# Optimization experiments

Hardware: AMD Instinct MI355X
Metric: run time of the kernel (lower is better)

Reference implementation:

```python
import jax, jax.numpy as jnp
import numpy as np

NUM_HEADS = 12

def _get_rel_pos(size, rel_pos):
    # q_size == k_size == size, no interpolation needed (table has 2*size-1 rows)
    idx = jnp.arange(size)[:, None] - jnp.arange(size)[None, :] + (size - 1)  # (size,size)
    return rel_pos[idx]  # (size, size, head_dim)

def setup_inputs() -> dict:
    key = jax.random.key(0)
    ks = jax.random.split(key, 7)
    B, H, W, dim = 8, 32, 32, 768
    head_dim = dim // NUM_HEADS
    return {
        "x": jax.random.normal(ks[0], (B, H, W, dim), jnp.float32),
        "qkv_w": jax.random.normal(ks[1], (dim, 3 * dim), jnp.float32) * 0.02,
        "qkv_b": jax.random.normal(ks[2], (3 * dim,), jnp.float32) * 0.02,
        "proj_w": jax.random.normal(ks[3], (dim, dim), jnp.float32) * 0.02,
        "proj_b": jax.random.normal(ks[4], (dim,), jnp.float32) * 0.02,
        "rel_pos_h": jax.random.normal(ks[5], (2 * H - 1, head_dim), jnp.float32) * 0.02,
        "rel_pos_w": jax.random.normal(ks[6], (2 * W - 1, head_dim), jnp.float32) * 0.02,
    }

def reference(x, qkv_w, qkv_b, proj_w, proj_b, rel_pos_h, rel_pos_w):
    B, H, W, dim = x.shape
    N = H * W
    head_dim = dim // NUM_HEADS
    scale = head_dim ** (-0.5)

    qkv = x.reshape(B, N, dim) @ qkv_w + qkv_b                     # (B,N,3*dim)
    qkv = qkv.reshape(B, N, 3, NUM_HEADS, head_dim)
    qkv = qkv.transpose(2, 0, 3, 1, 4).reshape(3, B * NUM_HEADS, N, head_dim)
    q, k, v = qkv[0], qkv[1], qkv[2]                               # (B*h, N, hd)

    attn = jnp.einsum("bnd,bmd->bnm", q * scale, k)                # (B*h, N, N)

    # decomposed relative position bias
    Rh = _get_rel_pos(H, rel_pos_h)                                # (H,H,hd)
    Rw = _get_rel_pos(W, rel_pos_w)                                # (W,W,hd)
    r_q = q.reshape(B * NUM_HEADS, H, W, head_dim)
    rel_h = jnp.einsum("bhwc,hkc->bhwk", r_q, Rh)                  # (B*h,H,W,H)
    rel_w = jnp.einsum("bhwc,wkc->bhwk", r_q, Rw)                  # (B*h,H,W,W)
    attn = (attn.reshape(B * NUM_HEADS, H, W, H, W)
            + rel_h[:, :, :, :, None]
            + rel_w[:, :, :, None, :]).reshape(B * NUM_HEADS, N, N)

    attn = jax.nn.softmax(attn, axis=-1)
    out = jnp.einsum("bnm,bmd->bnd", attn, v)                      # (B*h, N, hd)
    out = out.reshape(B, NUM_HEADS, H, W, head_dim).transpose(0, 2, 3, 1, 4).reshape(B, H, W, dim)
    return out @ proj_w + proj_b
```

## Files before the change

### kernel.cpp

```cpp
#include <hip/hip_runtime.h>
#include <hip/hip_bf16.h>
#include <math.h>

#define DIM   768
#define NHEAD 12
#define NQ    1024

typedef short  short8  __attribute__((ext_vector_type(8)));
typedef unsigned short us8 __attribute__((ext_vector_type(8)));
typedef float  f32x16  __attribute__((ext_vector_type(16)));

#if __has_builtin(__builtin_amdgcn_exp2f)
#define EXP2(x) __builtin_amdgcn_exp2f(x)
#else
#define EXP2(x) __expf(0.69314718056f * (x))
#endif
#define LOG2E 1.44269504089f

__device__ inline ushort f2b(float f) {
  union { float f; unsigned u; } c; c.f = f;
  unsigned r = (c.u + 0x7FFFu + ((c.u >> 16) & 1u)) >> 16;
  return (ushort)r;
}
__device__ inline float b2f(ushort h) {
  union { unsigned u; float f; } c; c.u = ((unsigned)h) << 16;
  return c.f;
}
__device__ inline ushort4 cvt4(float4 v) {
  ushort4 o; o.x = f2b(v.x); o.y = f2b(v.y); o.z = f2b(v.z); o.w = f2b(v.w);
  return o;
}

__global__ __launch_bounds__(256) void prep(
    const float* __restrict__ x, const float* __restrict__ qkv_w,
    const float* __restrict__ proj_w, ushort* __restrict__ Xb,
    ushort* __restrict__ Wqt, ushort* __restrict__ Wpt) {
  __shared__ ushort Ts[64][68];
  const int blk = blockIdx.x, tid = threadIdx.x;
  if (blk < 768) {
    const float4* src = (const float4*)x;
    ushort4* dst = (ushort4*)Xb;
    int base = blk * 2048;
#pragma unroll
    for (int it = 0; it < 8; ++it) {
      int i = base + it * 256 + tid;
      dst[i] = cvt4(src[i]);
    }
    return;
  }
  const float* W; ushort* Wt; int ncols, tk, tn;
  if (blk < 1200) { int t = blk - 768;  W = qkv_w; Wt = Wqt; ncols = 2304; tk = t % 12; tn = t / 12; }
  else            { int t = blk - 1200; W = proj_w; Wt = Wpt; ncols = 768; tk = t % 12; tn = t / 12; }
  const int kb = tk * 64, nb = tn * 64;
#pragma unroll
  for (int rr = 0; rr < 4; ++rr) {
    int r = (tid >> 4) + rr * 16, c4 = (tid & 15) * 4;
    float4 w = *(const float4*)(W + (size_t)(kb + r) * ncols + nb + c4);
    *(ushort4*)&Ts[r][c4] = cvt4(w);
  }
  __syncthreads();
#pragma unroll
  for (int wwi = 0; wwi < 2; ++wwi) {
    int n = (tid >> 3) + wwi * 32, k8 = (tid & 7) * 8;
    us8 v;
#pragma unroll
    for (int j = 0; j < 8; ++j) v[j] = Ts[k8 + j][n];
    *(us8*)(Wt + (size_t)(nb + n) * 768 + kb + k8) = v;
  }
}

template <int OUTBF>
__global__ __launch_bounds__(256, 2) void gemm_mfma(
    const ushort* __restrict__ A, const ushort* __restrict__ BT,
    const float* __restrict__ bias, void* __restrict__ Cp, int Nc) {
  __shared__ ushort Asl[128][72];
  __shared__ ushort Bsl[128][72];
  const int tid = threadIdx.x;
  const int bm = blockIdx.y * 128, bn = blockIdx.x * 128;
  const int lane = tid & 63, wv = tid >> 6;
  const int l31 = lane & 31, lh = lane >> 5;
  const int wm = (wv >> 1) * 64, wn = (wv & 1) * 64;

  f32x16 acc[2][2];
#pragma unroll
  for (int i = 0; i < 2; ++i)
#pragma unroll
    for (int j = 0; j < 2; ++j)
#pragma unroll
      for (int r = 0; r < 16; ++r) acc[i][j][r] = 0.f;

  for (int kt = 0; kt < 768; kt += 64) {
    __syncthreads();
#pragma unroll
    for (int it = 0; it < 4; ++it) {
      int item = tid + 256 * it;
      int r = item >> 3, c8 = (item & 7) * 8;
      *(us8*)&Asl[r][c8] = *(const us8*)(A + (size_t)(bm + r) * 768 + kt + c8);
      *(us8*)&Bsl[r][c8] = *(const us8*)(BT + (size_t)(bn + r) * 768 + kt + c8);
    }
    __syncthreads();
#pragma unroll
    for (int ks = 0; ks < 4; ++ks) {
      short8 a0 = *(const short8*)&Asl[wm + l31][ks * 16 + lh * 8];
      short8 a1 = *(const short8*)&Asl[wm + 32 + l31][ks * 16 + lh * 8];
      short8 b0 = *(const short8*)&Bsl[wn + l31][ks * 16 + lh * 8];
      short8 b1 = *(const short8*)&Bsl[wn + 32 + l31][ks * 16 + lh * 8];
      acc[0][0] = __builtin_amdgcn_mfma_f32_32x32x16_bf16(a0, b0, acc[0][0], 0, 0, 0);
      acc[0][1] = __builtin_amdgcn_mfma_f32_32x32x16_bf16(a0, b1, acc[0][1], 0, 0, 0);
      acc[1][0] = __builtin_amdgcn_mfma_f32_32x32x16_bf16(a1, b0, acc[1][0], 0, 0, 0);
      acc[1][1] = __builtin_amdgcn_mfma_f32_32x32x16_bf16(a1, b1, acc[1][1], 0, 0, 0);
    }
  }

#pragma unroll
  for (int mb = 0; mb < 2; ++mb)
#pragma unroll
    for (int nb = 0; nb < 2; ++nb) {
      int col = bn + wn + nb * 32 + l31;
      float bv = bias[col];
#pragma unroll
      for (int reg = 0; reg < 16; ++reg) {
        int row = bm + wm + mb * 32 + (reg & 3) + 8 * (reg >> 2) + 4 * lh;
        float o = acc[mb][nb][reg] + bv;
        if (OUTBF) ((ushort*)Cp)[(size_t)row * Nc + col] = f2b(o);
        else       ((float*)Cp)[(size_t)row * Nc + col] = o;
      }
    }
}

__global__ __launch_bounds__(256) void bias_kernel(
    const ushort* __restrict__ QKV, const float* __restrict__ rph,
    const float* __restrict__ rpw, ushort* __restrict__ RH,
    ushort* __restrict__ RW) {
  __shared__ ushort Qb[128][72];
  __shared__ ushort Tb[63][72];

  const int tid = threadIdx.x;
  const int bh = blockIdx.x;
  const int gy = blockIdx.y;
  const int b = bh / NHEAD, h = bh % NHEAD;
  const bool isH = gy < 8;
  const int g4 = isH ? gy : (gy - 8);
  const int lane = tid & 63, wv = tid >> 6;
  const int l31 = lane & 31, lh = lane >> 5;

  const ushort* qb = QKV + (size_t)b * NQ * 2304 + h * 64;
  const float* tab = isH ? rph : rpw;

#pragma unroll
  for (int it = 0; it < 4; ++it) {
    int item = tid + 256 * it;
    if (item < 63 * 16) {
      int r = item >> 4, q4 = (item & 15) * 4;
      float4 v = *(const float4*)(tab + r * 64 + q4);
      *(ushort4*)&Tb[r][q4] = cvt4(v);
    }
  }
#pragma unroll
  for (int it = 0; it < 4; ++it) {
    int item = tid + 256 * it;
    int r = item >> 3, c8 = (item & 7) * 8;
    int n = isH ? (g4 * 128 + r) : ((r & 31) * 32 + g4 * 4 + (r >> 5));
    *(us8*)&Qb[r][c8] = *(const us8*)(qb + (size_t)n * 2304 + c8);
  }
  __syncthreads();

  const int fixed = g4 * 4 + wv;
  f32x16 acc;
#pragma unroll
  for (int i = 0; i < 16; ++i) acc[i] = 0.f;
#pragma unroll
  for (int ks = 0; ks < 4; ++ks) {
    short8 a  = *(const short8*)&Qb[wv * 32 + l31][ks * 16 + lh * 8];
    short8 bb = *(const short8*)&Tb[fixed + 31 - l31][ks * 16 + lh * 8];
    acc = __builtin_amdgcn_mfma_f32_32x32x16_bf16(a, bb, acc, 0, 0, 0);
  }
  ushort* outp = isH ? RH : RW;
#pragma unroll
  for (int reg = 0; reg < 16; ++reg) {
    int row = (reg & 3) + 8 * (reg >> 2) + 4 * lh;
    int n = isH ? (fixed * 32 + row) : (row * 32 + fixed);
    outp[((size_t)bh * NQ + n) * 32 + l31] = f2b(acc[reg] * LOG2E);
  }
}

__global__ __launch_bounds__(256, 3) void attn_mfma(
    const ushort* __restrict__ QKV, const ushort* __restrict__ RH,
    const ushort* __restrict__ RW, ushort* __restrict__ O) {
  __shared__ ushort Qs[128][72];
  __shared__ ushort Ks[64][72];
  __shared__ ushort VT[64][72];
  __shared__ ushort Pb[128][40];
  __shared__ float  rhs2[2][128];

  const int tid = threadIdx.x;
  const int bh = blockIdx.x % 96;
  const int qt = blockIdx.x / 96;
  const int b = bh / NHEAD, h = bh % NHEAD;
  const int n0 = qt * 128;
  const int lane = tid & 63, wv = tid >> 6;
  const int l31 = lane & 31, lh = lane >> 5;
  const int wb = wv * 32;

  const ushort* qb = QKV + (size_t)b * NQ * 2304 + h * 64;
  const ushort* kb = qb + DIM;
  const ushort* vb = qb + 2 * DIM;

#pragma unroll
  for (int it = 0; it < 4; ++it) {
    int item = tid + 256 * it;
    int r = item >> 3, c8 = (item & 7) * 8;
    *(us8*)&Qs[r][c8] = *(const us8*)(qb + (size_t)(n0 + r) * 2304 + c8);
  }
  const ushort* rwp = RW + (size_t)bh * NQ * 32;
  float rwv[16];
#pragma unroll
  for (int reg = 0; reg < 16; ++reg) {
    int row = (reg & 3) + 8 * (reg >> 2) + 4 * lh;
    rwv[reg] = b2f(rwp[(size_t)(n0 + wb + row) * 32 + l31]);
  }
  const ushort* rhp = RH + (size_t)bh * NQ * 32;

  __syncthreads();
  short8 aq[4];
#pragma unroll
  for (int ks = 0; ks < 4; ++ks)
    aq[ks] = *(const short8*)&Qs[wb + l31][ks * 16 + lh * 8];

  f32x16 oacc0, oacc1;
#pragma unroll
  for (int i = 0; i < 16; ++i) { oacc0[i] = 0.f; oacc1[i] = 0.f; }
  float lacc[16];
#pragma unroll
  for (int i = 0; i < 16; ++i) lacc[i] = 0.f;

  for (int kt = 0; kt < NQ; kt += 64) {
    __syncthreads();
#pragma unroll
    for (int it = 0; it < 2; ++it) {
      int item = tid + 256 * it;
      int r = item >> 3, c8 = (item & 7) * 8;
      *(us8*)&Ks[r][c8] = *(const us8*)(kb + (size_t)(kt + r) * 2304 + c8);
    }
#pragma unroll
    for (int it = 0; it < 2; ++it) {
      int item = tid + 256 * it;
      int p = item & 31, d4 = (item >> 5) * 4;
      ushort4 v0 = *(const ushort4*)(vb + (size_t)(kt + 2 * p) * 2304 + d4);
      ushort4 v1 = *(const ushort4*)(vb + (size_t)(kt + 2 * p + 1) * 2304 + d4);
      *(unsigned*)&VT[d4 + 0][2 * p] = (unsigned)v0.x | ((unsigned)v1.x << 16);
      *(unsigned*)&VT[d4 + 1][2 * p] = (unsigned)v0.y | ((unsigned)v1.y << 16);
      *(unsigned*)&VT[d4 + 2][2 * p] = (unsigned)v0.z | ((unsigned)v1.z << 16);
      *(unsigned*)&VT[d4 + 3][2 * p] = (unsigned)v0.w | ((unsigned)v1.w << 16);
    }
    {
      int c = tid & 1, r = tid >> 1;
      rhs2[c][r] = b2f(rhp[(size_t)(n0 + r) * 32 + (kt >> 5) + c]);
    }
    __syncthreads();

#pragma unroll
    for (int cb = 0; cb < 2; ++cb) {
      f32x16 s;
#pragma unroll
      for (int i = 0; i < 16; ++i) s[i] = 0.f;
#pragma unroll
      for (int ks = 0; ks < 4; ++ks) {
        short8 bk = *(const short8*)&Ks[cb * 32 + l31][ks * 16 + lh * 8];
        s = __builtin_amdgcn_mfma_f32_32x32x16_bf16(aq[ks], bk, s, 0, 0, 0);
      }
      const float* rhrow = &rhs2[cb][wb + 4 * lh];
#pragma unroll
      for (int g = 0; g < 4; ++g) {
        float4 rh4 = *(const float4*)(rhrow + 8 * g);
        float rhv[4] = {rh4.x, rh4.y, rh4.z, rh4.w};
#pragma unroll
        for (int i = 0; i < 4; ++i) {
          int reg = g * 4 + i;
          float p = EXP2(fmaf(s[reg], 0.18033688f, rhv[i]) + rwv[reg]);
          lacc[reg] += p;
          Pb[wb + i + 8 * g + 4 * lh][l31] = f2b(p);
        }
      }
#pragma unroll
      for (int ks = 0; ks < 2; ++ks) {
        short8 ap  = *(const short8*)&Pb[wb + l31][ks * 16 + lh * 8];
        short8 bv0 = *(const short8*)&VT[l31][cb * 32 + ks * 16 + lh * 8];
        short8 bv1 = *(const short8*)&VT[32 + l31][cb * 32 + ks * 16 + lh * 8];
        oacc0 = __builtin_amdgcn_mfma_f32_32x32x16_bf16(ap, bv0, oacc0, 0, 0, 0);
        oacc1 = __builtin_amdgcn_mfma_f32_32x32x16_bf16(ap, bv1, oacc1, 0, 0, 0);
      }
    }
  }

  ushort* ob = O + ((size_t)b * NQ + n0 + wb) * DIM + h * 64;
#pragma unroll
  for (int reg = 0; reg < 16; ++reg) {
    float v = lacc[reg];
    v += __shfl_xor(v, 1);  v += __shfl_xor(v, 2);  v += __shfl_xor(v, 4);
    v += __shfl_xor(v, 8);  v += __shfl_xor(v, 16);
    float linv = 1.0f / v;
    int row = (reg & 3) + 8 * (reg >> 2) + 4 * lh;
    ob[(size_t)row * DIM + l31]      = f2b(oacc0[reg] * linv);
    ob[(size_t)row * DIM + 32 + l31] = f2b(oacc1[reg] * linv);
  }
}

extern "C" void kernel_launch(void* const* d_in, const int* in_sizes, int n_in,
                              void* d_out, int out_size, void* d_ws, size_t ws_size,
                              hipStream_t stream) {
  const float* x      = (const float*)d_in[0];
  const float* qkv_w  = (const float*)d_in[1];
  const float* qkv_b  = (const float*)d_in[2];
  const float* proj_w = (const float*)d_in[3];
  const float* proj_b = (const float*)d_in[4];
  const float* rel_h  = (const float*)d_in[5];
  const float* rel_w  = (const float*)d_in[6];
  float* out = (float*)d_out;

  ushort* qkvb = (ushort*)d_ws;
  ushort* obuf = qkvb + (size_t)8192 * 2304;
  ushort* RH   = obuf + (size_t)8192 * DIM;
  ushort* RW   = RH + (size_t)96 * NQ * 32;
  ushort* Xb   = RW + (size_t)96 * NQ * 32;
  ushort* Wqt  = Xb + (size_t)8192 * DIM;
  ushort* Wpt  = Wqt + (size_t)2304 * DIM;

  prep<<<dim3(1344), 256, 0, stream>>>(x, qkv_w, proj_w, Xb, Wqt, Wpt);

  gemm_mfma<1><<<dim3(2304 / 128, 8192 / 128), 256, 0, stream>>>(
      Xb, Wqt, qkv_b, qkvb, 2304);

  bias_kernel<<<dim3(96, 16), 256, 0, stream>>>(qkvb, rel_h, rel_w, RH, RW);

  attn_mfma<<<dim3(96 * 8), 256, 0, stream>>>(qkvb, RH, RW, obuf);

  gemm_mfma<0><<<dim3(768 / 128, 8192 / 128), 256, 0, stream>>>(
      obuf, Wpt, proj_b, out, 768);
}
```

Before: 227.6 us.

## Compute transposed S tile so each lane owns one query row

Swaps the MFMA operands so the score tile is computed as S^T, which gives each lane a single query row. The rel_h bias can then be read straight from global memory into registers, the row sum becomes one scalar per lane, and P is written to LDS as packed 8-byte stores. The shared rhs2 staging and the separate Pb buffer go away, with P reusing the Qs region per wave, which cuts LDS footprint and shuffle reductions. The risk is that reusing Qs for P is only safe because Q has already been copied into registers, and the final normalisation now needs per-row lane shuffles.

```diff
diff --git a/kernel.cpp b/kernel.cpp
--- a/kernel.cpp
+++ b/kernel.cpp
@@ -29,6 +29,9 @@
 __device__ inline ushort4 cvt4(float4 v) {
   ushort4 o; o.x = f2b(v.x); o.y = f2b(v.y); o.z = f2b(v.z); o.w = f2b(v.w);
   return o;
+}
+__device__ inline unsigned pkf(float a, float b) {
+  return (unsigned)f2b(a) | ((unsigned)f2b(b) << 16);
 }
 
 __global__ __launch_bounds__(256) void prep(
@@ -190,8 +193,6 @@
   __shared__ ushort Qs[128][72];
   __shared__ ushort Ks[64][72];
   __shared__ ushort VT[64][72];
-  __shared__ ushort Pb[128][40];
-  __shared__ float  rhs2[2][128];
 
   const int tid = threadIdx.x;
   const int bh = blockIdx.x % 96;
@@ -212,14 +213,17 @@
     int r = item >> 3, c8 = (item & 7) * 8;
     *(us8*)&Qs[r][c8] = *(const us8*)(qb + (size_t)(n0 + r) * 2304 + c8);
   }
-  const ushort* rwp = RW + (size_t)bh * NQ * 32;
+
+  const int q = n0 + wb + l31;
+  const ushort* rwrow = RW + ((size_t)bh * NQ + q) * 32;
   float rwv[16];
 #pragma unroll
-  for (int reg = 0; reg < 16; ++reg) {
-    int row = (reg & 3) + 8 * (reg >> 2) + 4 * lh;
-    rwv[reg] = b2f(rwp[(size_t)(n0 + wb + row) * 32 + l31]);
-  }
-  const ushort* rhp = RH + (size_t)bh * NQ * 32;
+  for (int g = 0; g < 4; ++g) {
+    ushort4 v = *(const ushort4*)(rwrow + 8 * g + 4 * lh);
+    rwv[4 * g + 0] = b2f(v.x); rwv[4 * g + 1] = b2f(v.y);
+    rwv[4 * g + 2] = b2f(v.z); rwv[4 * g + 3] = b2f(v.w);
+  }
+  const ushort* rhrow = RH + ((size_t)bh * NQ + q) * 32;
 
   __syncthreads();
   short8 aq[4];
@@ -227,15 +231,17 @@
   for (int ks = 0; ks < 4; ++ks)
     aq[ks] = *(const short8*)&Qs[wb + l31][ks * 16 + lh * 8];
 
+  ushort* Pb2 = &Qs[0][0] + wv * (32 * 40);
+
   f32x16 oacc0, oacc1;
 #pragma unroll
   for (int i = 0; i < 16; ++i) { oacc0[i] = 0.f; oacc1[i] = 0.f; }
-  float lacc[16];
-#pragma unroll
-  for (int i = 0; i < 16; ++i) lacc[i] = 0.f;
-
-  for (int kt = 0; kt < NQ; kt += 64) {
+  float lacc = 0.f;
+
+  for (int t = 0; t < 16; ++t) {
+    const int kt = t * 64;
     __syncthreads();
+    const unsigned rhu = *(const unsigned*)(rhrow + 2 * t);
 #pragma unroll
     for (int it = 0; it < 2; ++it) {
       int item = tid + 256 * it;
@@ -253,11 +259,10 @@
       *(unsigned*)&VT[d4 + 2][2 * p] = (unsigned)v0.z | ((unsigned)v1.z << 16);
       *(unsigned*)&VT[d4 + 3][2 * p] = (unsigned)v0.w | ((unsigned)v1.w << 16);
     }
-    {
-      int c = tid & 1, r = tid >> 1;
-      rhs2[c][r] = b2f(rhp[(size_t)(n0 + r) * 32 + (kt >> 5) + c]);
-    }
     __syncthreads();
+
+    const float rh0 = b2f((ushort)(rhu & 0xFFFF));
+    const float rh1 = b2f((ushort)(rhu >> 16));
 
 #pragma unroll
     for (int cb = 0; cb < 2; ++cb) {
@@ -266,25 +271,23 @@
       for (int i = 0; i < 16; ++i) s[i] = 0.f;
 #pragma unroll
       for (int ks = 0; ks < 4; ++ks) {
-        short8 bk = *(const short8*)&Ks[cb * 32 + l31][ks * 16 + lh * 8];
-        s = __builtin_amdgcn_mfma_f32_32x32x16_bf16(aq[ks], bk, s, 0, 0, 0);
+        short8 ak = *(const short8*)&Ks[cb * 32 + l31][ks * 16 + lh * 8];
+        s = __builtin_amdgcn_mfma_f32_32x32x16_bf16(ak, aq[ks], s, 0, 0, 0);
       }
-      const float* rhrow = &rhs2[cb][wb + 4 * lh];
+      const float rhv = cb ? rh1 : rh0;
 #pragma unroll
       for (int g = 0; g < 4; ++g) {
-        float4 rh4 = *(const float4*)(rhrow + 8 * g);
-        float rhv[4] = {rh4.x, rh4.y, rh4.z, rh4.w};
-#pragma unroll
-        for (int i = 0; i < 4; ++i) {
-          int reg = g * 4 + i;
-          float p = EXP2(fmaf(s[reg], 0.18033688f, rhv[i]) + rwv[reg]);
-          lacc[reg] += p;
-          Pb[wb + i + 8 * g + 4 * lh][l31] = f2b(p);
-        }
+        float p0 = EXP2(fmaf(s[4 * g + 0], 0.18033688f, rwv[4 * g + 0] + rhv));
+        float p1 = EXP2(fmaf(s[4 * g + 1], 0.18033688f, rwv[4 * g + 1] + rhv));
+        float p2 = EXP2(fmaf(s[4 * g + 2], 0.18033688f, rwv[4 * g + 2] + rhv));
+        float p3 = EXP2(fmaf(s[4 * g + 3], 0.18033688f, rwv[4 * g + 3] + rhv));
+        lacc += (p0 + p1) + (p2 + p3);
+        uint2 pk; pk.x = pkf(p0, p1); pk.y = pkf(p2, p3);
+        *(uint2*)&Pb2[l31 * 40 + 8 * g + 4 * lh] = pk;
       }
 #pragma unroll
       for (int ks = 0; ks < 2; ++ks) {
-        short8 ap  = *(const short8*)&Pb[wb + l31][ks * 16 + lh * 8];
+        short8 ap  = *(const short8*)&Pb2[l31 * 40 + ks * 16 + lh * 8];
         short8 bv0 = *(const short8*)&VT[l31][cb * 32 + ks * 16 + lh * 8];
         short8 bv1 = *(const short8*)&VT[32 + l31][cb * 32 + ks * 16 + lh * 8];
         oacc0 = __builtin_amdgcn_mfma_f32_32x32x16_bf16(ap, bv0, oacc0, 0, 0, 0);
@@ -293,16 +296,15 @@
     }
   }
 
+  lacc += __shfl_xor(lacc, 32);
+  const float linv = 1.0f / lacc;
   ushort* ob = O + ((size_t)b * NQ + n0 + wb) * DIM + h * 64;
 #pragma unroll
   for (int reg = 0; reg < 16; ++reg) {
-    float v = lacc[reg];
-    v += __shfl_xor(v, 1);  v += __shfl_xor(v, 2);  v += __shfl_xor(v, 4);
-    v += __shfl_xor(v, 8);  v += __shfl_xor(v, 16);
-    float linv = 1.0f / v;
     int row = (reg & 3) + 8 * (reg >> 2) + 4 * lh;
-    ob[(size_t)row * DIM + l31]      = f2b(oacc0[reg] * linv);
-    ob[(size_t)row * DIM + 32 + l31] = f2b(oacc1[reg] * linv);
+    float lq = __shfl(linv, row);
+    ob[(size_t)row * DIM + l31]      = f2b(oacc0[reg] * lq);
+    ob[(size_t)row * DIM + 32 + l31] = f2b(oacc1[reg] * lq);
   }
 }
 
```

Result: no change. 228.1 us (+0.2%).
